# Optimization experiments

Hardware: AMD Instinct MI355X
Metric: run time of the kernel (lower is better)

Reference implementation:

```python
import jax, jax.numpy as jnp
import numpy as np

B, S, P, L, SEQ, H = 16, 40, 512, 48, 2048, 1024


def setup_inputs() -> dict:
    rng = np.random.default_rng(0)
    # sentence lengths include the trailing separator token; tokens used per sentence = len - 1
    sentence_length = rng.integers(8, L + 1, size=(B, S)).astype(np.int32)
    passage_length = rng.integers(30, S + 1, size=(B,)).astype(np.int32)
    # valid pair ids must be < passage_length per example
    pairs_list = (rng.random((B, P, 2)) * passage_length[:, None, None]).astype(np.int32)
    pairs_num = rng.integers(256, P + 1, size=(B,)).astype(np.int32)
    key = jax.random.key(0)
    top_rep = jax.random.normal(key, (B, SEQ, H), dtype=jnp.float32)
    return {
        "sentence_length": jnp.asarray(sentence_length),
        "pairs_list": jnp.asarray(pairs_list),
        "passage_length": jnp.asarray(passage_length),
        "pairs_num": jnp.asarray(pairs_num),
        "max_sentence_length": L,
        "top_rep": top_rep,
    }


def reference(sentence_length, pairs_list, passage_length, pairs_num, max_sentence_length, top_rep):
    Bb, Ss = sentence_length.shape
    Pp = pairs_list.shape[1]
    Ll = int(max_sentence_length)
    seq = top_rep.shape[1]

    # tokens per sentence (sentence_length - 1), zeroed beyond passage_length
    sen_mask = jnp.arange(Ss)[None, :] < passage_length[:, None]          # [B,S]
    tok = jnp.where(sen_mask, sentence_length - 1, 0)                     # [B,S]
    # start offset of each sentence in top_rep (first token at index 1)
    starts = 1 + jnp.cumsum(tok, axis=1) - tok                            # [B,S] exclusive cumsum + 1

    t = jnp.arange(Ll)
    idx = jnp.clip(starts[:, :, None] + t[None, None, :], 0, seq - 1)     # [B,S,L]
    valid = t[None, None, :] < tok[:, :, None]                            # [B,S,L]
    sen_emb = top_rep[jnp.arange(Bb)[:, None, None], idx]                 # [B,S,L,H] gather
    sen_emb = jnp.where(valid[..., None], sen_emb, jnp.zeros((), top_rep.dtype))

    # pair cls = mean over concat(sent_i tokens, sent_j tokens) = (sum_i+sum_j)/(cnt_i+cnt_j)
    sent_sum = sen_emb.sum(axis=2)                                        # [B,S,H]
    cnt = tok.astype(top_rep.dtype)                                       # [B,S]

    p = jnp.clip(pairs_list, 0, Ss - 1)                                   # [B,P,2]
    s0 = jnp.take_along_axis(sent_sum, p[:, :, 0][:, :, None], axis=1)    # [B,P,H]
    s1 = jnp.take_along_axis(sent_sum, p[:, :, 1][:, :, None], axis=1)    # [B,P,H]
    c0 = jnp.take_along_axis(cnt, p[:, :, 0], axis=1)                     # [B,P]
    c1 = jnp.take_along_axis(cnt, p[:, :, 1], axis=1)
    denom = jnp.maximum(c0 + c1, 1.0)

    pair_mask = jnp.arange(Pp)[None, :] < pairs_num[:, None]              # [B,P]
    cls = jnp.where(pair_mask[..., None], (s0 + s1) / denom[..., None], 0.0)
    return sen_emb, cls[:, :, None, :]                                    # [B,S,L,H], [B,P,1,H]
```

## Files before the change

kernel.cpp:

```cpp
#include <hip/hip_runtime.h>
#include <hip/hip_bf16.h>

#define CB   16
#define CS   40
#define CP   512
#define CL   48
#define CSEQ 2048
#define CH   1024
#define H4   (CH / 4)

typedef float fvec4 __attribute__((ext_vector_type(4)));

__global__ void __launch_bounds__(256)
gather_kernel(const float* __restrict__ top_rep,
              const int* __restrict__ sentence_length,
              const int* __restrict__ passage_length,
              float* __restrict__ sen_emb,
              float* __restrict__ sent_sum) {
    const int bs   = blockIdx.x;
    const int b    = bs / CS;
    const int s    = bs - b * CS;
    const int h4   = threadIdx.x;
    const int lane = threadIdx.x & 63;

    const int pl = passage_length[b];
    int tokl = 0;
    if (lane < CS && lane < pl) tokl = sentence_length[b * CS + lane] - 1;
    int x = tokl;
    #pragma unroll
    for (int off = 1; off < 64; off <<= 1) {
        int y = __shfl_up(x, off);
        if (lane >= off) x += y;
    }
    const int tok   = __shfl(tokl, s);
    const int start = 1 + __shfl(x, s) - tok;

    const fvec4* __restrict__ rep =
        reinterpret_cast<const fvec4*>(top_rep) + (size_t)b * CSEQ * H4;
    fvec4* __restrict__ out =
        reinterpret_cast<fvec4*>(sen_emb) + (size_t)bs * CL * H4;

    fvec4 acc = {0.f, 0.f, 0.f, 0.f};

    #pragma unroll 4
    for (int t = 0; t < CL; ++t) {
        fvec4 v = {0.f, 0.f, 0.f, 0.f};
        if (t < tok) {
            int row = start + t;
            row = min(max(row, 0), CSEQ - 1);
            v = rep[(size_t)row * H4 + h4];
        }
        __builtin_nontemporal_store(v, &out[(size_t)t * H4 + h4]);
        acc += v;
    }

    reinterpret_cast<fvec4*>(sent_sum)[(size_t)bs * H4 + h4] = acc;
}

__global__ void __launch_bounds__(256)
cls_kernel(const int* __restrict__ pairs_list,
           const int* __restrict__ pairs_num,
           const int* __restrict__ sentence_length,
           const int* __restrict__ passage_length,
           const float* __restrict__ sent_sum,
           float* __restrict__ cls) {
    const int blk = blockIdx.x;
    const int b   = blk / CP;
    const int i   = blk - b * CP;
    const int h4  = threadIdx.x;

    fvec4 r = {0.f, 0.f, 0.f, 0.f};

    if (i < pairs_num[b]) {
        int p0 = pairs_list[(size_t)blk * 2 + 0];
        int p1 = pairs_list[(size_t)blk * 2 + 1];
        p0 = min(max(p0, 0), CS - 1);
        p1 = min(max(p1, 0), CS - 1);

        const int pl = passage_length[b];
        const float c0 = (p0 < pl) ? (float)(sentence_length[b * CS + p0] - 1) : 0.f;
        const float c1 = (p1 < pl) ? (float)(sentence_length[b * CS + p1] - 1) : 0.f;
        const float denom = fmaxf(c0 + c1, 1.0f);

        const fvec4* __restrict__ ss = reinterpret_cast<const fvec4*>(sent_sum);
        fvec4 a0 = ss[(size_t)(b * CS + p0) * H4 + h4];
        fvec4 a1 = ss[(size_t)(b * CS + p1) * H4 + h4];

        r = (a0 + a1) / denom;
    }

    __builtin_nontemporal_store(
        r, &reinterpret_cast<fvec4*>(cls)[(size_t)blk * H4 + h4]);
}

extern "C" void kernel_launch(void* const* d_in, const int* in_sizes, int n_in,
                              void* d_out, int out_size, void* d_ws, size_t ws_size,
                              hipStream_t stream) {
    const int*   sentence_length = (const int*)  d_in[0];
    const int*   pairs_list      = (const int*)  d_in[1];
    const int*   passage_length  = (const int*)  d_in[2];
    const int*   pairs_num       = (const int*)  d_in[3];
    const float* top_rep         = (const float*)d_in[5];

    float* out     = (float*)d_out;
    float* sen_emb = out;
    float* cls     = out + (size_t)CB * CS * CL * CH;

    float* sent_sum = (float*)d_ws;

    gather_kernel<<<CB * CS, 256, 0, stream>>>(
        top_rep, sentence_length, passage_length, sen_emb, sent_sum);

    cls_kernel<<<CB * CP, 256, 0, stream>>>(
        pairs_list, pairs_num, sentence_length, passage_length, sent_sum, cls);
}
```

Measured before the change: 42.23 us.

## Split sentence-sum pass from output emission so sen_emb and cls writes share one launch

The first kernel now only computes per-sentence sums without writing sen_emb. A second kernel covers both sentence blocks, which write the padded sen_emb tiles by re-gathering rows, and pair blocks, which write cls, so the large output writes overlap with the cls work in a single grid. The cost is reading the gathered top_rep rows twice, and the sen_emb writes still wait behind the first kernel. The loop unroll factor is also raised from 4 to 8.

```diff
diff --git a/kernel.cpp b/kernel.cpp
--- a/kernel.cpp
+++ b/kernel.cpp
@@ -8,21 +8,15 @@
 #define CSEQ 2048
 #define CH   1024
 #define H4   (CH / 4)
+#define NSENT (CB * CS)
+#define NPAIR (CB * CP)
 
 typedef float fvec4 __attribute__((ext_vector_type(4)));
 
-__global__ void __launch_bounds__(256)
-gather_kernel(const float* __restrict__ top_rep,
-              const int* __restrict__ sentence_length,
-              const int* __restrict__ passage_length,
-              float* __restrict__ sen_emb,
-              float* __restrict__ sent_sum) {
-    const int bs   = blockIdx.x;
-    const int b    = bs / CS;
-    const int s    = bs - b * CS;
-    const int h4   = threadIdx.x;
-    const int lane = threadIdx.x & 63;
-
+__device__ __forceinline__ void sentence_meta(
+    const int* __restrict__ sentence_length,
+    const int* __restrict__ passage_length,
+    int b, int s, int lane, int& tok, int& start) {
     const int pl = passage_length[b];
     int tokl = 0;
     if (lane < CS && lane < pl) tokl = sentence_length[b * CS + lane] - 1;
@@ -32,65 +26,103 @@
         int y = __shfl_up(x, off);
         if (lane >= off) x += y;
     }
-    const int tok   = __shfl(tokl, s);
-    const int start = 1 + __shfl(x, s) - tok;
+    tok   = __shfl(tokl, s);
+    start = 1 + __shfl(x, s) - tok;
+}
+
+__global__ void __launch_bounds__(256)
+sum_kernel(const float* __restrict__ top_rep,
+           const int* __restrict__ sentence_length,
+           const int* __restrict__ passage_length,
+           float* __restrict__ sent_sum) {
+    const int bs   = blockIdx.x;
+    const int b    = bs / CS;
+    const int s    = bs - b * CS;
+    const int h4   = threadIdx.x;
+    const int lane = threadIdx.x & 63;
+
+    int tok, start;
+    sentence_meta(sentence_length, passage_length, b, s, lane, tok, start);
 
     const fvec4* __restrict__ rep =
         reinterpret_cast<const fvec4*>(top_rep) + (size_t)b * CSEQ * H4;
-    fvec4* __restrict__ out =
-        reinterpret_cast<fvec4*>(sen_emb) + (size_t)bs * CL * H4;
 
     fvec4 acc = {0.f, 0.f, 0.f, 0.f};
 
-    #pragma unroll 4
+    #pragma unroll 8
     for (int t = 0; t < CL; ++t) {
-        fvec4 v = {0.f, 0.f, 0.f, 0.f};
         if (t < tok) {
             int row = start + t;
             row = min(max(row, 0), CSEQ - 1);
-            v = rep[(size_t)row * H4 + h4];
+            acc += rep[(size_t)row * H4 + h4];
         }
-        __builtin_nontemporal_store(v, &out[(size_t)t * H4 + h4]);
-        acc += v;
     }
 
     reinterpret_cast<fvec4*>(sent_sum)[(size_t)bs * H4 + h4] = acc;
 }
 
 __global__ void __launch_bounds__(256)
-cls_kernel(const int* __restrict__ pairs_list,
-           const int* __restrict__ pairs_num,
-           const int* __restrict__ sentence_length,
-           const int* __restrict__ passage_length,
-           const float* __restrict__ sent_sum,
-           float* __restrict__ cls) {
-    const int blk = blockIdx.x;
-    const int b   = blk / CP;
-    const int i   = blk - b * CP;
-    const int h4  = threadIdx.x;
+emit_kernel(const float* __restrict__ top_rep,
+            const int* __restrict__ sentence_length,
+            const int* __restrict__ passage_length,
+            const int* __restrict__ pairs_list,
+            const int* __restrict__ pairs_num,
+            const float* __restrict__ sent_sum,
+            float* __restrict__ sen_emb,
+            float* __restrict__ cls) {
+    const int k    = blockIdx.x;
+    const int h4   = threadIdx.x;
+    const int lane = threadIdx.x & 63;
 
-    fvec4 r = {0.f, 0.f, 0.f, 0.f};
+    if (k < NSENT) {
+        const int b = k / CS;
+        const int s = k - b * CS;
 
-    if (i < pairs_num[b]) {
-        int p0 = pairs_list[(size_t)blk * 2 + 0];
-        int p1 = pairs_list[(size_t)blk * 2 + 1];
-        p0 = min(max(p0, 0), CS - 1);
-        p1 = min(max(p1, 0), CS - 1);
+        int tok, start;
+        sentence_meta(sentence_length, passage_length, b, s, lane, tok, start);
 
-        const int pl = passage_length[b];
-        const float c0 = (p0 < pl) ? (float)(sentence_length[b * CS + p0] - 1) : 0.f;
-        const float c1 = (p1 < pl) ? (float)(sentence_length[b * CS + p1] - 1) : 0.f;
-        const float denom = fmaxf(c0 + c1, 1.0f);
+        const fvec4* __restrict__ rep =
+            reinterpret_cast<const fvec4*>(top_rep) + (size_t)b * CSEQ * H4;
+        fvec4* __restrict__ out =
+            reinterpret_cast<fvec4*>(sen_emb) + (size_t)k * CL * H4;
 
-        const fvec4* __restrict__ ss = reinterpret_cast<const fvec4*>(sent_sum);
-        fvec4 a0 = ss[(size_t)(b * CS + p0) * H4 + h4];
-        fvec4 a1 = ss[(size_t)(b * CS + p1) * H4 + h4];
+        #pragma unroll 8
+        for (int t = 0; t < CL; ++t) {
+            fvec4 v = {0.f, 0.f, 0.f, 0.f};
+            if (t < tok) {
+                int row = start + t;
+                row = min(max(row, 0), CSEQ - 1);
+                v = rep[(size_t)row * H4 + h4];
+            }
+            __builtin_nontemporal_store(v, &out[(size_t)t * H4 + h4]);
+        }
+    } else {
+        const int j = k - NSENT;
+        const int b = j >> 9;
+        const int i = j & (CP - 1);
 
-        r = (a0 + a1) / denom;
+        fvec4 r = {0.f, 0.f, 0.f, 0.f};
+
+        if (i < pairs_num[b]) {
+            int p0 = pairs_list[(size_t)j * 2 + 0];
+            int p1 = pairs_list[(size_t)j * 2 + 1];
+            p0 = min(max(p0, 0), CS - 1);
+            p1 = min(max(p1, 0), CS - 1);
+
+            const int pl = passage_length[b];
+            const float c0 = (p0 < pl) ? (float)(sentence_length[b * CS + p0] - 1) : 0.f;
+            const float c1 = (p1 < pl) ? (float)(sentence_length[b * CS + p1] - 1) : 0.f;
+            const float denom = fmaxf(c0 + c1, 1.0f);
+
+            const fvec4* __restrict__ ss = reinterpret_cast<const fvec4*>(sent_sum);
+            fvec4 a0 = ss[(size_t)(b * CS + p0) * H4 + h4];
+            fvec4 a1 = ss[(size_t)(b * CS + p1) * H4 + h4];
+            r = (a0 + a1) / denom;
+        }
+
+        __builtin_nontemporal_store(
+            r, &reinterpret_cast<fvec4*>(cls)[(size_t)j * H4 + h4]);
     }
-
-    __builtin_nontemporal_store(
-        r, &reinterpret_cast<fvec4*>(cls)[(size_t)blk * H4 + h4]);
 }
 
 extern "C" void kernel_launch(void* const* d_in, const int* in_sizes, int n_in,
@@ -108,9 +140,10 @@
 
     float* sent_sum = (float*)d_ws;
 
-    gather_kernel<<<CB * CS, 256, 0, stream>>>(
-        top_rep, sentence_length, passage_length, sen_emb, sent_sum);
+    sum_kernel<<<NSENT, 256, 0, stream>>>(
+        top_rep, sentence_length, passage_length, sent_sum);
 
-    cls_kernel<<<CB * CP, 256, 0, stream>>>(
-        pairs_list, pairs_num, sentence_length, passage_length, sent_sum, cls);
+    emit_kernel<<<NSENT + NPAIR, 256, 0, stream>>>(
+        top_rep, sentence_length, passage_length, pairs_list, pairs_num,
+        sent_sum, sen_emb, cls);
 }
```

After: 57.17 us. 35.4% more time.
